# Kernel tuning notes

Measured on AMD Instinct MI355X. Metric: run time of the kernel, lower is better.

Reference implementation:

```python
import jax, jax.numpy as jnp
import numpy as np

NF = 64            # n_filter
CFAC = 3           # SinSobel c_factor: identity + sobel-x + sobel-y
FIN = NF * CFAC    # dyna block input channels (192)
FH = NF * 2        # dyna hidden (128)
FOUT = NF          # dyna output (64)
LAT = 512
N_CALLS = 6        # ceil(log2(128) - log2(2))
P_SIZES = [FH * FIN, FH, FH * FH, FH, FOUT * FH, FOUT, FOUT * FIN, FOUT]
P_TOTAL = sum(P_SIZES)  # 61824
_OFFS = np.cumsum([0] + P_SIZES)

def act(t):
    return jax.nn.leaky_relu(t, 0.2)

def conv1x1(x, w, b):
    # x [B,I,H,W], w [O,I] -> [B,O,H,W]
    return jnp.einsum('bihw,oi->bohw', x, w) + b[None, :, None, None]

def res_block(x, w0, b0, w1, b1):
    # GAN-stability style residual block with 1x1 convs
    return x + 0.1 * conv1x1(act(conv1x1(act(x), w0, b0)), w1, b1)

def depthwise3x3(x, k2d):
    C = x.shape[1]
    k = jnp.broadcast_to(k2d.astype(x.dtype), (C, 1, 3, 3))
    return jax.lax.conv_general_dilated(
        x, k, (1, 1), [(1, 1), (1, 1)],
        dimension_numbers=('NCHW', 'OIHW', 'NCHW'),
        feature_group_count=C)

SOBEL_X = jnp.array([[1., 0., -1.], [2., 0., -2.], [1., 0., -1.]], jnp.float32) / 8.0
SOBEL_Y = SOBEL_X.T
_g = jnp.exp(-0.5 * jnp.array([-1., 0., 1.], jnp.float32) ** 2)
GAUSS = jnp.outer(_g, _g)
GAUSS = GAUSS / GAUSS.sum()

def sin_sobel(x):
    return jnp.concatenate([x, depthwise3x3(x, SOBEL_X), depthwise3x3(x, SOBEL_Y)], axis=1)

def dyna_residual(x, params):
    # per-sample hypernetwork-generated 1x1-conv residual block
    B = x.shape[0]
    def take(i, shape):
        return params[:, _OFFS[i]:_OFFS[i + 1]].reshape((B,) + shape)
    w_in, b_in = take(0, (FH, FIN)), take(1, (FH,))
    w_mid, b_mid = take(2, (FH, FH)), take(3, (FH,))
    w_out, b_out = take(4, (FOUT, FH)), take(5, (FOUT,))
    w_sk, b_sk = take(6, (FOUT, FIN)), take(7, (FOUT,))
    def pconv(h, w, b):  # batched per-sample 1x1 conv
        return jnp.einsum('bihw,boi->bohw', h, w) + b[:, :, None, None]
    x_s = pconv(x, w_sk, b_sk)
    dx = pconv(x, w_in, b_in)
    dx = pconv(act(dx), w_mid, b_mid)
    dx = pconv(act(dx), w_out, b_out)
    return x_s + dx

def downsample(x):
    # GaussianSmoothing(k=3, sigma=1, pad=1) then bilinear 0.5
    # (align_corners=False bilinear at scale 0.5 == 2x2 average pooling)
    x = depthwise3x3(x, GAUSS)
    B, C, H, W = x.shape
    return x.reshape(B, C, H // 2, 2, W // 2, 2).mean(axis=(3, 5))

def lin_res(x, w1, b1, w2, b2, sw=None, sb=None):
    x_s = x if sw is None else x @ sw + sb
    return x_s + 0.1 * (act(act(x) @ w1 + b1) @ w2 + b2)

def forward(x, inj_lat, leak, in_w, in_b, inrb_w0, inrb_b0, inrb_w1, inrb_b1,
            hyp_w, hyp_b, outrb_w0, outrb_b0, outrb_w1, outrb_b1,
            l1_sw, l1_sb, l1_w1, l1_b1, l1_w2, l1_b2,
            l2_w1, l2_b1, l2_w2, l2_b2, lo_w, lo_b):
    out = conv1x1(x, in_w, in_b)
    out = res_block(out, inrb_w0, inrb_b0, inrb_w1, inrb_b1)
    leak_f = jnp.clip(leak, 0.001, 1000.0)
    dyn_params = inj_lat @ hyp_w + hyp_b  # [B, P_TOTAL], shared across calls
    out_embs = [out]
    for _ in range(N_CALLS):  # fixed small layer loop; spatial dims halve each call
        out_new = sin_sobel(out)
        out_new = dyna_residual(out_new, dyn_params)
        out = out + leak_f * out_new
        out = downsample(out)
        out_embs.append(out)
    out = res_block(out, outrb_w0, outrb_b0, outrb_w1, outrb_b1)
    h = out.mean(axis=(2, 3))  # [B, NF]
    h = lin_res(h, l1_w1, l1_b1, l1_w2, l1_b2, l1_sw, l1_sb)
    h = lin_res(h, l2_w1, l2_b1, l2_w2, l2_b2)
    lat = h @ lo_w + lo_b
    return lat, out_embs

def setup_inputs() -> dict:
    key = jax.random.key(0)
    ks = jax.random.split(key, 24)
    B, C, S = 8, 3, 128
    def rn(k, shape, scale=0.05):
        return scale * jax.random.normal(k, shape, jnp.float32)
    z = lambda n: jnp.zeros((n,), jnp.float32)
    return {
        'x': jax.random.normal(ks[0], (B, C, S, S), jnp.float32),
        'inj_lat': jax.random.normal(ks[1], (B, LAT), jnp.float32),
        'leak': jnp.array(0.1, jnp.float32),
        'in_w': rn(ks[2], (NF, C)), 'in_b': z(NF),
        'inrb_w0': rn(ks[3], (NF, NF)), 'inrb_b0': z(NF),
        'inrb_w1': rn(ks[4], (NF, NF)), 'inrb_b1': z(NF),
        'hyp_w': rn(ks[5], (LAT, P_TOTAL), 0.01), 'hyp_b': rn(ks[6], (P_TOTAL,), 0.01),
        'outrb_w0': rn(ks[7], (NF, NF)), 'outrb_b0': z(NF),
        'outrb_w1': rn(ks[8], (NF, NF)), 'outrb_b1': z(NF),
        'l1_sw': rn(ks[9], (NF, LAT)), 'l1_sb': z(LAT),
        'l1_w1': rn(ks[10], (NF, 2 * LAT)), 'l1_b1': z(2 * LAT),
        'l1_w2': rn(ks[11], (2 * LAT, LAT)), 'l1_b2': z(LAT),
        'l2_w1': rn(ks[12], (LAT, LAT)), 'l2_b1': z(LAT),
        'l2_w2': rn(ks[13], (LAT, LAT)), 'l2_b2': z(LAT),
        'lo_w': rn(ks[14], (LAT, LAT)), 'lo_b': z(LAT),
    }

def reference(x, inj_lat, leak, in_w, in_b, inrb_w0, inrb_b0, inrb_w1, inrb_b1,
              hyp_w, hyp_b, outrb_w0, outrb_b0, outrb_w1, outrb_b1,
              l1_sw, l1_sb, l1_w1, l1_b1, l1_w2, l1_b2,
              l2_w1, l2_b1, l2_w2, l2_b2, lo_w, lo_b):
    lat, out_embs = forward(x, inj_lat, leak, in_w, in_b, inrb_w0, inrb_b0, inrb_w1, inrb_b1,
                            hyp_w, hyp_b, outrb_w0, outrb_b0, outrb_w1, outrb_b1,
                            l1_sw, l1_sb, l1_w1, l1_b1, l1_w2, l1_b2,
                            l2_w1, l2_b1, l2_w2, l2_b2, lo_w, lo_b)
    return (lat, *out_embs)
```

## Files before the change

kernel.cpp:

```cpp
#include <hip/hip_runtime.h>


#define BATCH 8
#define PT 61824

typedef __attribute__((ext_vector_type(8))) short bf16x8;
typedef __attribute__((ext_vector_type(4))) float f32x4;

__device__ __forceinline__ float lrelu(float v) { return v > 0.f ? v : 0.2f * v; }

__device__ __forceinline__ unsigned cvt_pk_bf16(float lo, float hi) {
    unsigned r;
    asm("v_cvt_pk_bf16_f32 %0, %1, %2" : "=v"(r) : "v"(lo), "v"(hi));
    return r;
}
__device__ __forceinline__ short f2bf1(float f) {
    unsigned r;
    asm("v_cvt_pk_bf16_f32 %0, %1, %1" : "=v"(r) : "v"(f));
    return (short)r;
}

__global__ __launch_bounds__(256) void hyper_kernel(
    const float* __restrict__ inj, const float* __restrict__ hw,
    const float* __restrict__ hb, float* __restrict__ dyn,
    short* __restrict__ dyn16)
{
    __shared__ float s_l[512 * 8];
    __shared__ float s_part[3 * 8 * 64];
    int t = threadIdx.x;
    for (int i = t; i < 4096; i += 256) {
        int b = i >> 9, k = i & 511;
        s_l[k * 8 + b] = inj[i];
    }
    __syncthreads();
    int po = t & 63, kq = t >> 6;
    int p = blockIdx.x * 64 + po;
    float acc[8];
#pragma unroll
    for (int b = 0; b < 8; ++b) acc[b] = 0.f;
    for (int k = kq * 128; k < kq * 128 + 128; ++k) {
        float w = hw[(size_t)k * PT + p];
        float4 a0 = *(const float4*)&s_l[k * 8];
        float4 a1 = *(const float4*)&s_l[k * 8 + 4];
        acc[0] += a0.x * w; acc[1] += a0.y * w; acc[2] += a0.z * w; acc[3] += a0.w * w;
        acc[4] += a1.x * w; acc[5] += a1.y * w; acc[6] += a1.z * w; acc[7] += a1.w * w;
    }
    if (kq > 0) {
#pragma unroll
        for (int b = 0; b < 8; ++b) s_part[((kq - 1) * 8 + b) * 64 + po] = acc[b];
    }
    __syncthreads();
    if (kq == 0) {
        float bias = hb[p];
        bool isb = (p >= 24576 && p < 24704) || (p >= 41088 && p < 41216)
                || (p >= 49408 && p < 49472) || (p >= 61760);
#pragma unroll
        for (int b = 0; b < 8; ++b) {
            float v = acc[b] + s_part[b * 64 + po] + s_part[(8 + b) * 64 + po]
                    + s_part[(16 + b) * 64 + po] + bias;
            if (isb) dyn[(size_t)b * PT + p] = v;
            dyn16[(size_t)b * PT + p] = f2bf1(v);
        }
    }
}

__global__ __launch_bounds__(256) void stem_kernel(
    const float* __restrict__ x, const float* __restrict__ in_w,
    const float* __restrict__ in_b,
    const float* __restrict__ w0, const float* __restrict__ b0,
    const float* __restrict__ w1, const float* __restrict__ b1,
    float* __restrict__ out0)
{
    const int HW = 128 * 128;
    __shared__ float s_t0[64 * 68];
    __shared__ short s_vh[2 * 64 * 72];
    __shared__ float s_x[192];
    short* s_v = s_vh;
    short* s_h = s_vh + 64 * 72;
    float* s_y = (float*)s_vh;

    const int b = blockIdx.x >> 8;
    const int tile = blockIdx.x & 255;
    const int pix0 = tile * 64;
    const int t = threadIdx.x;
    const int l = t & 63, w = t >> 6;
    const int lp = l & 15, lq = l >> 4;

    if (t < 192) s_x[t] = x[(size_t)b * 3 * HW + (t >> 6) * HW + pix0 + (t & 63)];
    __syncthreads();

    for (int j = t; j < 1024; j += 256) {
        int p = j & 63, cg = j >> 6;
        float x0 = s_x[p], x1 = s_x[64 + p], x2 = s_x[128 + p];
        short pk[4];
#pragma unroll
        for (int cc = 0; cc < 4; ++cc) {
            int c = cg * 4 + cc;
            float v = in_b[c] + x0 * in_w[c * 3] + x1 * in_w[c * 3 + 1]
                    + x2 * in_w[c * 3 + 2];
            s_t0[c * 68 + p] = v;
            pk[cc] = f2bf1(lrelu(v));
        }
        *(short4*)&s_v[p * 72 + cg * 4] = make_short4(pk[0], pk[1], pk[2], pk[3]);
    }
    __syncthreads();

    const int o = w * 16 + lp;
    const f32x4 z4 = {0.f, 0.f, 0.f, 0.f};

    bf16x8 wb0[2], wb1[2];
#pragma unroll
    for (int k = 0; k < 2; ++k) {
        bf16x8 p0, p1;
#pragma unroll
        for (int e = 0; e < 8; ++e) {
            p0[e] = f2bf1(w0[o * 64 + k * 32 + lq * 8 + e]);
            p1[e] = f2bf1(w1[o * 64 + k * 32 + lq * 8 + e]);
        }
        wb0[k] = p0; wb1[k] = p1;
    }

    {
        float bi = b0[o];
        f32x4 acc[4];
#pragma unroll
        for (int mt = 0; mt < 4; ++mt) acc[mt] = z4;
#pragma unroll
        for (int k = 0; k < 2; ++k)
#pragma unroll
            for (int mt = 0; mt < 4; ++mt) {
                bf16x8 a = *(const bf16x8*)&s_v[(mt * 16 + lp) * 72 + k * 32 + lq * 8];
                acc[mt] = __builtin_amdgcn_mfma_f32_16x16x32_bf16(a, wb0[k], acc[mt], 0, 0, 0);
            }
#pragma unroll
        for (int mt = 0; mt < 4; ++mt)
#pragma unroll
            for (int r = 0; r < 4; ++r)
                s_h[(mt * 16 + lq * 4 + r) * 72 + o] = f2bf1(lrelu(acc[mt][r] + bi));
    }
    __syncthreads();

    {
        float bi = b1[o];
        f32x4 acc[4];
#pragma unroll
        for (int mt = 0; mt < 4; ++mt) acc[mt] = z4;
#pragma unroll
        for (int k = 0; k < 2; ++k)
#pragma unroll
            for (int mt = 0; mt < 4; ++mt) {
                bf16x8 a = *(const bf16x8*)&s_h[(mt * 16 + lp) * 72 + k * 32 + lq * 8];
                acc[mt] = __builtin_amdgcn_mfma_f32_16x16x32_bf16(a, wb1[k], acc[mt], 0, 0, 0);
            }
        __syncthreads();
#pragma unroll
        for (int mt = 0; mt < 4; ++mt) {
            f32x4 dv;
#pragma unroll
            for (int r = 0; r < 4; ++r) dv[r] = 0.1f * (acc[mt][r] + bi);
            *(f32x4*)&s_y[o * 68 + mt * 16 + lq * 4] = dv;
        }
    }
    __syncthreads();

#pragma unroll
    for (int v = 0; v < 4; ++v) {
        int idx = v * 1024 + t * 4;
        int oo = idx >> 6, px = idx & 63;
        f32x4 t0v = *(const f32x4*)&s_t0[oo * 68 + px];
        f32x4 dv = *(const f32x4*)&s_y[oo * 68 + px];
        f32x4 ov = t0v + dv;
        *(f32x4*)&out0[((size_t)b * 64 + oo) * HW + pix0 + px] = ov;
    }
}

template<int MT>
__global__ __launch_bounds__(256)
__attribute__((amdgpu_waves_per_eu(4, 4)))
void iter_kernel(
    const float* __restrict__ cur, const float* __restrict__ dynf,
    const short* __restrict__ dynb, const float* __restrict__ leak_p,
    float* __restrict__ y, int S, int sh)
{
    constexpr int PX = MT * 16;
    constexpr int SY = (MT == 4) ? 68 : 20;
    __shared__ short s_s[PX * 192];
    __shared__ short s_h[PX * 128];
    float* s_y = (float*)s_s;

    const int HW = S * S;
    const int tilesPer = HW / PX;
    const int nwg = BATCH * tilesPer;
    const int rb = (int)blockIdx.x;
    const int lb = (rb & 7) * (nwg >> 3) + (rb >> 3);
    const int b = lb / tilesPer;
    const int tile = lb - b * tilesPer;
    const int pix0 = tile * PX;
    const int t = threadIdx.x;
    const int l = t & 63, w = t >> 6;
    const int lp = l & 15, lq = l >> 4;
    const float* base = cur + (size_t)b * 64 * HW;
    const float lk = fminf(fmaxf(leak_p[0], 0.001f), 1000.f);

    if constexpr (MT == 4) {
        const int p = lp + 16 * w;
        const int rxw = (p & 7) << 2;
        const int gpx = pix0 + p;
        const int row = gpx >> sh;
        const int x = gpx & (S - 1);
        const bool rm = (row > 0), rp = (row < S - 1);
        float* halo_a = (float*)s_h;
        float* halo_d = halo_a + 640;
        int* s32 = (int*)s_s;

        float vm[16], vv[16], vp[16];
        const float* col = base + row * S + x;
#pragma unroll
        for (int j = 0; j < 16; ++j) {
            const int c = 2 * (lq + 4 * (j >> 1)) + (j & 1);
            const float* ch = col + (size_t)c * HW;
            vm[j] = rm ? ch[-S] : 0.f;
            vv[j] = ch[0];
            vp[j] = rp ? ch[S] : 0.f;
        }
        __builtin_amdgcn_sched_barrier(0);
        float a[16], d[16];
#pragma unroll
        for (int j = 0; j < 16; ++j) {
            a[j] = vm[j] + 2.f * vv[j] + vp[j];
            d[j] = vm[j] - vp[j];
        }
        if (w == 0 || w == 3) {
            const bool left = (w == 0) && (lp == 0);
            const bool right = (w == 3) && (lp == 15);
            if (left || right) {
                const int xe = left ? x - 1 : x + 1;
                const int slot = left ? 8 : 9;
                const bool valid = (xe >= 0) && (xe < S);
                const float* ecol = base + row * S + xe;
#pragma unroll
                for (int j = 0; j < 16; ++j) {
                    const int c = 2 * (lq + 4 * (j >> 1)) + (j & 1);
                    float em = 0.f, e0 = 0.f, ep = 0.f;
                    if (valid) {
                        const float* ch = ecol + (size_t)c * HW;
                        em = rm ? ch[-S] : 0.f;
                        e0 = ch[0];
                        ep = rp ? ch[S] : 0.f;
                    }
                    halo_a[slot * 64 + c] = em + 2.f * e0 + ep;
                    halo_d[slot * 64 + c] = em - ep;
                }
            }
        }
        if (lp == 0 || lp == 15) {
            const int slot = 2 * w + (lp == 15 ? 1 : 0);
#pragma unroll
            for (int j = 0; j < 16; ++j) {
                const int c = 2 * (lq + 4 * (j >> 1)) + (j & 1);
                halo_a[slot * 64 + c] = a[j];
                halo_d[slot * 64 + c] = d[j];
            }
        }
        __syncthreads();
        const int slotL = (w == 0) ? 8 : 2 * (w - 1) + 1;
        const int slotR = (w == 3) ? 9 : 2 * (w + 1);
#pragma unroll
        for (int i = 0; i < 8; ++i) {
            float sx2[2], sy2[2];
#pragma unroll
            for (int cc = 0; cc < 2; ++cc) {
                const int j = 2 * i + cc;
                const int c = 2 * (lq + 4 * i) + cc;
                float aL = __shfl(a[j], l - 1), dL = __shfl(d[j], l - 1);
                float aR = __shfl(a[j], l + 1), dR = __shfl(d[j], l + 1);
                if (lp == 0)  { aL = halo_a[slotL * 64 + c]; dL = halo_d[slotL * 64 + c]; }
                if (lp == 15) { aR = halo_a[slotR * 64 + c]; dR = halo_d[slotR * 64 + c]; }
                if (x == 0)     { aL = 0.f; dL = 0.f; }
                if (x == S - 1) { aR = 0.f; dR = 0.f; }
                sx2[cc] = (aL - aR) * 0.125f;
                sy2[cc] = (dL + 2.f * d[j] + dR) * 0.125f;
            }
            const int cp = lq + 4 * i;
            const int cpx_ = cp ^ rxw;
            s32[p * 96 + cpx_] = (int)cvt_pk_bf16(vv[2 * i], vv[2 * i + 1]);
            s32[p * 96 + 32 + cpx_] = (int)cvt_pk_bf16(sx2[0], sx2[1]);
            s32[p * 96 + 64 + cpx_] = (int)cvt_pk_bf16(sy2[0], sy2[1]);
        }
    } else {
        const int p = lp;
        const int rxw = (p & 7) << 2;
        const int gpx = pix0 + p;
        const int row = gpx >> sh;
        const int x = gpx & (S - 1);
        const bool rm = (row > 0), rp = (row < S - 1);
        const bool le = (lp == 0) && (x > 0);
        const bool re = (lp == 15) && (x < S - 1);
        int* s32 = (int*)s_s;
#pragma unroll
        for (int i = 0; i < 2; ++i) {
            const int cp = lq + 4 * w + 16 * i;
            float v0s[2], sxs[2], sys[2];
#pragma unroll
            for (int cc = 0; cc < 2; ++cc) {
                const int c = 2 * cp + cc;
                const float* ch = base + (size_t)c * HW + row * S;
                float vm = rm ? ch[x - S] : 0.f;
                float v0 = ch[x];
                float vp = rp ? ch[x + S] : 0.f;
                float elm = 0.f, el0 = 0.f, elp = 0.f, erm = 0.f, er0 = 0.f, erp = 0.f;
                if (le) { elm = rm ? ch[x - 1 - S] : 0.f; el0 = ch[x - 1]; elp = rp ? ch[x - 1 + S] : 0.f; }
                if (re) { erm = rm ? ch[x + 1 - S] : 0.f; er0 = ch[x + 1]; erp = rp ? ch[x + 1 + S] : 0.f; }
                float Lm = __shfl(vm, l - 1), L0 = __shfl(v0, l - 1), Lp = __shfl(vp, l - 1);
                float Rm = __shfl(vm, l + 1), R0 = __shfl(v0, l + 1), Rp = __shfl(vp, l + 1);
                if (lp == 0)  { Lm = elm; L0 = el0; Lp = elp; }
                if (lp == 15) { Rm = erm; R0 = er0; Rp = erp; }
                if (x == 0)     { Lm = 0.f; L0 = 0.f; Lp = 0.f; }
                if (x == S - 1) { Rm = 0.f; R0 = 0.f; Rp = 0.f; }
                v0s[cc] = v0;
                sxs[cc] = (Lm - Rm + 2.f * (L0 - R0) + Lp - Rp) * 0.125f;
                sys[cc] = (Lm + 2.f * vm + Rm - Lp - 2.f * vp - Rp) * 0.125f;
            }
            const int cpx_ = cp ^ rxw;
            s32[p * 96 + cpx_] = (int)cvt_pk_bf16(v0s[0], v0s[1]);
            s32[p * 96 + 32 + cpx_] = (int)cvt_pk_bf16(sxs[0], sxs[1]);
            s32[p * 96 + 64 + cpx_] = (int)cvt_pk_bf16(sys[0], sys[1]);
        }
    }
    __syncthreads();

    const short* wb = dynb + (size_t)b * PT;
    const float* pf = dynf + (size_t)b * PT;
    const f32x4 z4 = {0.f, 0.f, 0.f, 0.f};
    const int sx4 = (lp & 7) << 4;
    const char* ss_b = (const char*)s_s;
    const char* sh_cb = (const char*)s_h;
    char* sh_b = (char*)s_h;

    f32x4 acc_sk[MT];
#pragma unroll
    for (int mt = 0; mt < MT; ++mt) acc_sk[mt] = z4;

    {
        const float bi0 = pf[24576 + (w * 2) * 16 + lp];
        const float bi1 = pf[24576 + (w * 2 + 1) * 16 + lp];
        f32x4 acc[2][MT];
#pragma unroll
        for (int n = 0; n < 2; ++n)
#pragma unroll
            for (int mt = 0; mt < MT; ++mt) acc[n][mt] = z4;
        const int osk = w * 16 + lp;
        __builtin_amdgcn_s_setprio(1);
#pragma unroll 2
        for (int k = 0; k < 6; ++k) {
            bf16x8 a[MT];
#pragma unroll
            for (int mt = 0; mt < MT; ++mt)
                a[mt] = *(const bf16x8*)(ss_b + (mt * 16 + lp) * 384 + ((k * 64 + lq * 16) ^ sx4));
#pragma unroll
            for (int n = 0; n < 2; ++n) {
                int o = (w * 2 + n) * 16 + lp;
                bf16x8 bb = *(const bf16x8*)&wb[o * 192 + k * 32 + lq * 8];
#pragma unroll
                for (int mt = 0; mt < MT; ++mt)
                    acc[n][mt] = __builtin_amdgcn_mfma_f32_16x16x32_bf16(a[mt], bb, acc[n][mt], 0, 0, 0);
            }
            {
                bf16x8 bsk = *(const bf16x8*)&wb[49472 + osk * 192 + k * 32 + lq * 8];
#pragma unroll
                for (int mt = 0; mt < MT; ++mt)
                    acc_sk[mt] = __builtin_amdgcn_mfma_f32_16x16x32_bf16(a[mt], bsk, acc_sk[mt], 0, 0, 0);
            }
        }
        __builtin_amdgcn_s_setprio(0);
#pragma unroll
        for (int n = 0; n < 2; ++n) {
            int o = (w * 2 + n) * 16 + lp;
            float bi = n ? bi1 : bi0;
#pragma unroll
            for (int mt = 0; mt < MT; ++mt)
#pragma unroll
                for (int r = 0; r < 4; ++r) {
                    int row = mt * 16 + lq * 4 + r;
                    *(short*)(sh_b + row * 256 + ((o * 2) ^ ((row & 7) << 4))) =
                        f2bf1(lrelu(acc[n][mt][r] + bi));
                }
        }
    }
    __syncthreads();

    {
        const float bi0 = pf[41088 + (w * 2) * 16 + lp];
        const float bi1 = pf[41088 + (w * 2 + 1) * 16 + lp];
        f32x4 acc[2][MT];
#pragma unroll
        for (int n = 0; n < 2; ++n)
#pragma unroll
            for (int mt = 0; mt < MT; ++mt) acc[n][mt] = z4;
#pragma unroll 2
        for (int k = 0; k < 4; ++k) {
            bf16x8 a[MT];
#pragma unroll
            for (int mt = 0; mt < MT; ++mt)
                a[mt] = *(const bf16x8*)(sh_cb + (mt * 16 + lp) * 256 + ((k * 64 + lq * 16) ^ sx4));
#pragma unroll
            for (int n = 0; n < 2; ++n) {
                int o = (w * 2 + n) * 16 + lp;
                bf16x8 bb = *(const bf16x8*)&wb[24704 + o * 128 + k * 32 + lq * 8];
#pragma unroll
                for (int mt = 0; mt < MT; ++mt)
                    acc[n][mt] = __builtin_amdgcn_mfma_f32_16x16x32_bf16(a[mt], bb, acc[n][mt], 0, 0, 0);
            }
        }
        __syncthreads();
#pragma unroll
        for (int n = 0; n < 2; ++n) {
            int o = (w * 2 + n) * 16 + lp;
            float bi = n ? bi1 : bi0;
#pragma unroll
            for (int mt = 0; mt < MT; ++mt)
#pragma unroll
                for (int r = 0; r < 4; ++r) {
                    int row = mt * 16 + lq * 4 + r;
                    *(short*)(sh_b + row * 256 + ((o * 2) ^ ((row & 7) << 4))) =
                        f2bf1(lrelu(acc[n][mt][r] + bi));
                }
        }
    }
    __syncthreads();

    {
        int o = w * 16 + lp;
        const float bi = pf[49408 + o] + pf[61760 + o];
        f32x4 acc[MT];
#pragma unroll
        for (int mt = 0; mt < MT; ++mt) acc[mt] = acc_sk[mt];
#pragma unroll 2
        for (int k = 0; k < 4; ++k) {
            bf16x8 bb = *(const bf16x8*)&wb[41216 + o * 128 + k * 32 + lq * 8];
#pragma unroll
            for (int mt = 0; mt < MT; ++mt) {
                bf16x8 a = *(const bf16x8*)(sh_cb + (mt * 16 + lp) * 256 + ((k * 64 + lq * 16) ^ sx4));
                acc[mt] = __builtin_amdgcn_mfma_f32_16x16x32_bf16(a, bb, acc[mt], 0, 0, 0);
            }
        }
#pragma unroll
        for (int mt = 0; mt < MT; ++mt) {
            f32x4 dv;
#pragma unroll
            for (int r = 0; r < 4; ++r) dv[r] = acc[mt][r] + bi;
            *(f32x4*)&s_y[o * SY + mt * 16 + lq * 4] = dv;
        }
    }
    __syncthreads();

    {
        if (MT == 4) {
#pragma unroll
            for (int v = 0; v < 4; ++v) {
                int idx = v * 1024 + t * 4;
                int o = idx >> 6, px = idx & 63;
                f32x4 sv = *(const f32x4*)&s_y[o * SY + px];
                const float* cb = cur + ((size_t)b * 64 + o) * HW + pix0 + px;
                float* yb = y + ((size_t)b * 64 + o) * HW + pix0 + px;
                f32x4 cv = *(const f32x4*)cb;
                *(f32x4*)yb = cv + lk * sv;
            }
        } else {
            int o = t >> 2, px = (t & 3) * 4;
            f32x4 sv = *(const f32x4*)&s_y[o * SY + px];
            const float* cb = cur + ((size_t)b * 64 + o) * HW + pix0 + px;
            float* yb = y + ((size_t)b * 64 + o) * HW + pix0 + px;
            f32x4 cv = *(const f32x4*)cb;
            *(f32x4*)yb = cv + lk * sv;
        }
    }
}

__global__ __launch_bounds__(256) void down_kernel(
    const float* __restrict__ yin, float* __restrict__ outp,
    int S, int S2, int TW, int CPB, int tiles)
{
    __shared__ float s_in[3072];
    __shared__ float s_hb[1152];

    const float ga = 0.60653065971263342f;
    const float gs = 1.f / ((1.f + 2.f * ga) * (1.f + 2.f * ga));
    const float u0 = ga, u1 = 1.f + ga;

    const int t = threadIdx.x;
    const int nwg = (int)gridDim.x;
    const int rb = (int)blockIdx.x;
    const int bi = (rb & 7) * (nwg >> 3) + (rb >> 3);
    const int tix = bi % tiles;
    const int rem = bi / tiles;
    const int tiy = rem % tiles;
    const int cg = rem / tiles;
    const int bc0 = cg * CPB;

    const int IH = 2 * TW + 2;
    const int IW = IH;
    const int IWP = IW + 2;
    const int HS = TW + 1;
    const int gy0 = tiy * 2 * TW - 1;
    const int gx0 = tix * 2 * TW - 1;

    const int loadTot = CPB * IH * IW;
    for (int j = t; j < loadTot; j += 256) {
        int c = j / (IH * IW);
        int r = j - c * (IH * IW);
        int iy = r / IW, ix = r - iy * IW;
        int gy = gy0 + iy, gx = gx0 + ix;
        float v = 0.f;
        if (gy >= 0 && gy < S && gx >= 0 && gx < S)
            v = yin[(size_t)(bc0 + c) * S * S + gy * S + gx];
        s_in[(c * IH + iy) * IWP + ix] = v;
    }
    __syncthreads();

    const int hTot = CPB * IH * TW;
    for (int j = t; j < hTot; j += 256) {
        int c = j / (IH * TW);
        int r = j - c * (IH * TW);
        int iy = r / TW, ox = r - iy * TW;
        const float* pin = &s_in[(c * IH + iy) * IWP + 2 * ox];
        s_hb[(c * IH + iy) * HS + ox] =
            u0 * (pin[0] + pin[3]) + u1 * (pin[1] + pin[2]);
    }
    __syncthreads();

    {
        int ox = t % TW;
        int r = t / TW;
        int oy = r % TW;
        int c = r / TW;
        const float* ph = &s_hb[(c * IH + 2 * oy) * HS + ox];
        float acc = u0 * (ph[0] + ph[3 * HS]) + u1 * (ph[HS] + ph[2 * HS]);
        outp[(size_t)(bc0 + c) * S2 * S2 + (tiy * TW + oy) * S2 + tix * TW + ox] =
            acc * 0.25f * gs;
    }
}

__global__ __launch_bounds__(256) void head_a_kernel(
    const float* __restrict__ emb6,
    const float* __restrict__ w0, const float* __restrict__ b0,
    const float* __restrict__ w1, const float* __restrict__ b1,
    float* __restrict__ h)
{
    __shared__ float sm_t[256], sm_v[256], sm_r[256];
    int b = blockIdx.x, t = threadIdx.x;
    sm_t[t] = emb6[b * 256 + t];
    __syncthreads();
    {
        int o = t & 63, p = t >> 6;
        float acc = 0.f;
        for (int k = 0; k < 64; ++k) acc += w0[o * 64 + k] * lrelu(sm_t[k * 4 + p]);
        sm_v[o * 4 + p] = lrelu(acc + b0[o]);
    }
    __syncthreads();
    {
        int o = t & 63, p = t >> 6;
        float acc = 0.f;
        for (int k = 0; k < 64; ++k) acc += w1[o * 64 + k] * sm_v[k * 4 + p];
        sm_r[o * 4 + p] = sm_t[o * 4 + p] + 0.1f * (acc + b1[o]);
    }
    __syncthreads();
    if (t < 64)
        h[b * 64 + t] = 0.25f * (sm_r[t * 4] + sm_r[t * 4 + 1] + sm_r[t * 4 + 2] + sm_r[t * 4 + 3]);
}

__global__ __launch_bounds__(256) void head_b_kernel(
    const float* __restrict__ h, const float* __restrict__ w,
    const float* __restrict__ bias, float* __restrict__ t1)
{
    __shared__ float s_h[64];
    int id = blockIdx.x * 256 + threadIdx.x;
    int b = id >> 10, o = id & 1023;
    if (threadIdx.x < 64) s_h[threadIdx.x] = lrelu(h[b * 64 + threadIdx.x]);
    __syncthreads();
    float acc = 0.f;
    for (int k = 0; k < 64; ++k) acc += s_h[k] * w[k * 1024 + o];
    t1[b * 1024 + o] = lrelu(acc + bias[o]);
}

__global__ __launch_bounds__(256) void head_c_kernel(
    const float* __restrict__ h, const float* __restrict__ t1,
    const float* __restrict__ sw, const float* __restrict__ sb,
    const float* __restrict__ w2, const float* __restrict__ b2,
    float* __restrict__ h1)
{
    __shared__ float s_t[8 * 128];
    __shared__ float s_h[8 * 64];
    int oblk = blockIdx.x & 1, chunk = blockIdx.x >> 1;
    int t = threadIdx.x;
    int o = oblk * 256 + t;
    for (int j = t; j < 1024; j += 256) {
        int b = j >> 7, kk = j & 127;
        s_t[j] = t1[b * 1024 + chunk * 128 + kk];
    }
    if (chunk == 0)
        for (int j = t; j < 512; j += 256) s_h[j] = h[j];
    __syncthreads();
    float acc[8];
#pragma unroll
    for (int b = 0; b < 8; ++b) acc[b] = 0.f;
    for (int kk = 0; kk < 128; ++kk) {
        float wv = w2[(chunk * 128 + kk) * 512 + o];
#pragma unroll
        for (int b = 0; b < 8; ++b) acc[b] += s_t[b * 128 + kk] * wv;
    }
#pragma unroll
    for (int b = 0; b < 8; ++b) acc[b] *= 0.1f;
    if (chunk == 0) {
        for (int k = 0; k < 64; ++k) {
            float wv = sw[k * 512 + o];
#pragma unroll
            for (int b = 0; b < 8; ++b) acc[b] += s_h[b * 64 + k] * wv;
        }
        float c0 = sb[o] + 0.1f * b2[o];
#pragma unroll
        for (int b = 0; b < 8; ++b) acc[b] += c0;
    }
#pragma unroll
    for (int b = 0; b < 8; ++b) atomicAdd(&h1[b * 512 + o], acc[b]);
}

__global__ __launch_bounds__(256) void head_d_kernel(
    const float* __restrict__ h1, const float* __restrict__ w,
    const float* __restrict__ bias, float* __restrict__ z3)
{
    __shared__ float s_u[8 * 64];
    int oblk = blockIdx.x & 1, chunk = blockIdx.x >> 1;
    int t = threadIdx.x;
    int o = oblk * 256 + t;
    for (int j = t; j < 512; j += 256) {
        int b = j >> 6, kk = j & 63;
        s_u[j] = lrelu(h1[b * 512 + chunk * 64 + kk]);
    }
    __syncthreads();
    float acc[8];
#pragma unroll
    for (int b = 0; b < 8; ++b) acc[b] = 0.f;
    for (int kk = 0; kk < 64; ++kk) {
        float wv = w[(chunk * 64 + kk) * 512 + o];
#pragma unroll
        for (int b = 0; b < 8; ++b) acc[b] += s_u[b * 64 + kk] * wv;
    }
    if (chunk == 0) {
        float c0 = bias[o];
#pragma unroll
        for (int b = 0; b < 8; ++b) acc[b] += c0;
    }
#pragma unroll
    for (int b = 0; b < 8; ++b) atomicAdd(&z3[b * 512 + o], acc[b]);
}

__global__ __launch_bounds__(256) void head_e_kernel(
    const float* __restrict__ h1, const float* __restrict__ z3,
    const float* __restrict__ w, const float* __restrict__ bias,
    float* __restrict__ h2)
{
    __shared__ float s_u[8 * 64];
    int oblk = blockIdx.x & 1, chunk = blockIdx.x >> 1;
    int t = threadIdx.x;
    int o = oblk * 256 + t;
    for (int j = t; j < 512; j += 256) {
        int b = j >> 6, kk = j & 63;
        s_u[j] = lrelu(z3[b * 512 + chunk * 64 + kk]);
    }
    __syncthreads();
    float acc[8];
#pragma unroll
    for (int b = 0; b < 8; ++b) acc[b] = 0.f;
    for (int kk = 0; kk < 64; ++kk) {
        float wv = w[(chunk * 64 + kk) * 512 + o];
#pragma unroll
        for (int b = 0; b < 8; ++b) acc[b] += s_u[b * 64 + kk] * wv;
    }
#pragma unroll
    for (int b = 0; b < 8; ++b) acc[b] *= 0.1f;
    if (chunk == 0) {
        float c0 = 0.1f * bias[o];
#pragma unroll
        for (int b = 0; b < 8; ++b) acc[b] += h1[b * 512 + o] + c0;
    }
#pragma unroll
    for (int b = 0; b < 8; ++b) atomicAdd(&h2[b * 512 + o], acc[b]);
}

__global__ __launch_bounds__(256) void head_f_kernel(
    const float* __restrict__ h2, const float* __restrict__ w,
    const float* __restrict__ bias, float* __restrict__ lat)
{
    __shared__ float s_u[8 * 64];
    int oblk = blockIdx.x & 1, chunk = blockIdx.x >> 1;
    int t = threadIdx.x;
    int o = oblk * 256 + t;
    for (int j = t; j < 512; j += 256) {
        int b = j >> 6, kk = j & 63;
        s_u[j] = h2[b * 512 + chunk * 64 + kk];
    }
    __syncthreads();
    float acc[8];
#pragma unroll
    for (int b = 0; b < 8; ++b) acc[b] = 0.f;
    for (int kk = 0; kk < 64; ++kk) {
        float wv = w[(chunk * 64 + kk) * 512 + o];
#pragma unroll
        for (int b = 0; b < 8; ++b) acc[b] += s_u[b * 64 + kk] * wv;
    }
    if (chunk == 0) {
        float c0 = bias[o];
#pragma unroll
        for (int b = 0; b < 8; ++b) acc[b] += c0;
    }
#pragma unroll
    for (int b = 0; b < 8; ++b) atomicAdd(&lat[b * 512 + o], acc[b]);
}

extern "C" void kernel_launch(void* const* d_in, const int* in_sizes, int n_in,
                              void* d_out, int out_size, void* d_ws, size_t ws_size,
                              hipStream_t stream) {
    const float* x      = (const float*)d_in[0];
    const float* inj    = (const float*)d_in[1];
    const float* leak   = (const float*)d_in[2];
    const float* in_w   = (const float*)d_in[3];
    const float* in_b   = (const float*)d_in[4];
    const float* inrb_w0 = (const float*)d_in[5];
    const float* inrb_b0 = (const float*)d_in[6];
    const float* inrb_w1 = (const float*)d_in[7];
    const float* inrb_b1 = (const float*)d_in[8];
    const float* hyp_w  = (const float*)d_in[9];
    const float* hyp_b  = (const float*)d_in[10];
    const float* outrb_w0 = (const float*)d_in[11];
    const float* outrb_b0 = (const float*)d_in[12];
    const float* outrb_w1 = (const float*)d_in[13];
    const float* outrb_b1 = (const float*)d_in[14];
    const float* l1_sw  = (const float*)d_in[15];
    const float* l1_sb  = (const float*)d_in[16];
    const float* l1_w1  = (const float*)d_in[17];
    const float* l1_b1  = (const float*)d_in[18];
    const float* l1_w2  = (const float*)d_in[19];
    const float* l1_b2  = (const float*)d_in[20];
    const float* l2_w1  = (const float*)d_in[21];
    const float* l2_b1  = (const float*)d_in[22];
    const float* l2_w2  = (const float*)d_in[23];
    const float* l2_b2  = (const float*)d_in[24];
    const float* lo_w   = (const float*)d_in[25];
    const float* lo_b   = (const float*)d_in[26];

    float* out = (float*)d_out;
    float* dyn = (float*)d_ws;
    float* ybuf = dyn + (size_t)BATCH * PT;
    short* dyn16 = (short*)(ybuf + (size_t)BATCH * 64 * 16384);
    float* hbuf = (float*)(dyn16 + (size_t)BATCH * PT);
    float* t1buf = hbuf + 512;
    float* h1buf = t1buf + 8192;
    float* z3buf = h1buf + 4096;
    float* h2buf = z3buf + 4096;

    hipMemsetAsync(h1buf, 0, (4096 * 3) * sizeof(float), stream);
    hipMemsetAsync(out, 0, 4096 * sizeof(float), stream);

    hyper_kernel<<<PT / 64, 256, 0, stream>>>(inj, hyp_w, hyp_b, dyn, dyn16);

    size_t cur = 4096;
    stem_kernel<<<BATCH * 256, 256, 0, stream>>>(
        x, in_w, in_b, inrb_w0, inrb_b0, inrb_w1, inrb_b1, out + cur);

    int S = 128, sh = 7;
    for (int i = 0; i < 6; ++i) {
        if (S >= 8) {
            iter_kernel<4><<<BATCH * (S * S / 64), 256, 0, stream>>>(
                out + cur, dyn, dyn16, leak, ybuf, S, sh);
        } else {
            iter_kernel<1><<<BATCH * (S * S / 16), 256, 0, stream>>>(
                out + cur, dyn, dyn16, leak, ybuf, S, sh);
        }
        int S2 = S >> 1;
        size_t nxt = cur + (size_t)BATCH * 64 * S * S;
        int TW = (S2 >= 16) ? 16 : S2;
        int tiles = S2 / TW;
        int CPB = 256 / (TW * TW);
        if (CPB < 1) CPB = 1;
        int grid = (BATCH * 64 / CPB) * tiles * tiles;
        down_kernel<<<grid, 256, 0, stream>>>(ybuf, out + nxt, S, S2, TW, CPB, tiles);
        cur = nxt;
        S = S2; sh -= 1;
    }

    head_a_kernel<<<BATCH, 256, 0, stream>>>(
        out + cur, outrb_w0, outrb_b0, outrb_w1, outrb_b1, hbuf);
    head_b_kernel<<<32, 256, 0, stream>>>(hbuf, l1_w1, l1_b1, t1buf);
    head_c_kernel<<<16, 256, 0, stream>>>(hbuf, t1buf, l1_sw, l1_sb, l1_w2, l1_b2, h1buf);
    head_d_kernel<<<16, 256, 0, stream>>>(h1buf, l2_w1, l2_b1, z3buf);
    head_e_kernel<<<16, 256, 0, stream>>>(h1buf, z3buf, l2_w2, l2_b2, h2buf);
    head_f_kernel<<<16, 256, 0, stream>>>(h2buf, lo_w, lo_b, out);
}
```

Measured before the change: 509.8 us.

## Merge hyper and stem kernels; fuse small-scale iterations and head into tail kernel

```diff
diff --git a/kernel.cpp b/kernel.cpp
--- a/kernel.cpp
+++ b/kernel.cpp
@@ -20,187 +20,22 @@
     return (short)r;
 }
 
-__global__ __launch_bounds__(256) void hyper_kernel(
-    const float* __restrict__ inj, const float* __restrict__ hw,
-    const float* __restrict__ hb, float* __restrict__ dyn,
-    short* __restrict__ dyn16)
-{
-    __shared__ float s_l[512 * 8];
-    __shared__ float s_part[3 * 8 * 64];
-    int t = threadIdx.x;
-    for (int i = t; i < 4096; i += 256) {
-        int b = i >> 9, k = i & 511;
-        s_l[k * 8 + b] = inj[i];
-    }
-    __syncthreads();
-    int po = t & 63, kq = t >> 6;
-    int p = blockIdx.x * 64 + po;
-    float acc[8];
-#pragma unroll
-    for (int b = 0; b < 8; ++b) acc[b] = 0.f;
-    for (int k = kq * 128; k < kq * 128 + 128; ++k) {
-        float w = hw[(size_t)k * PT + p];
-        float4 a0 = *(const float4*)&s_l[k * 8];
-        float4 a1 = *(const float4*)&s_l[k * 8 + 4];
-        acc[0] += a0.x * w; acc[1] += a0.y * w; acc[2] += a0.z * w; acc[3] += a0.w * w;
-        acc[4] += a1.x * w; acc[5] += a1.y * w; acc[6] += a1.z * w; acc[7] += a1.w * w;
-    }
-    if (kq > 0) {
-#pragma unroll
-        for (int b = 0; b < 8; ++b) s_part[((kq - 1) * 8 + b) * 64 + po] = acc[b];
-    }
-    __syncthreads();
-    if (kq == 0) {
-        float bias = hb[p];
-        bool isb = (p >= 24576 && p < 24704) || (p >= 41088 && p < 41216)
-                || (p >= 49408 && p < 49472) || (p >= 61760);
-#pragma unroll
-        for (int b = 0; b < 8; ++b) {
-            float v = acc[b] + s_part[b * 64 + po] + s_part[(8 + b) * 64 + po]
-                    + s_part[(16 + b) * 64 + po] + bias;
-            if (isb) dyn[(size_t)b * PT + p] = v;
-            dyn16[(size_t)b * PT + p] = f2bf1(v);
-        }
-    }
-}
-
-__global__ __launch_bounds__(256) void stem_kernel(
-    const float* __restrict__ x, const float* __restrict__ in_w,
-    const float* __restrict__ in_b,
-    const float* __restrict__ w0, const float* __restrict__ b0,
-    const float* __restrict__ w1, const float* __restrict__ b1,
-    float* __restrict__ out0)
-{
-    const int HW = 128 * 128;
-    __shared__ float s_t0[64 * 68];
-    __shared__ short s_vh[2 * 64 * 72];
-    __shared__ float s_x[192];
-    short* s_v = s_vh;
-    short* s_h = s_vh + 64 * 72;
-    float* s_y = (float*)s_vh;
-
-    const int b = blockIdx.x >> 8;
-    const int tile = blockIdx.x & 255;
-    const int pix0 = tile * 64;
-    const int t = threadIdx.x;
-    const int l = t & 63, w = t >> 6;
-    const int lp = l & 15, lq = l >> 4;
-
-    if (t < 192) s_x[t] = x[(size_t)b * 3 * HW + (t >> 6) * HW + pix0 + (t & 63)];
-    __syncthreads();
-
-    for (int j = t; j < 1024; j += 256) {
-        int p = j & 63, cg = j >> 6;
-        float x0 = s_x[p], x1 = s_x[64 + p], x2 = s_x[128 + p];
-        short pk[4];
-#pragma unroll
-        for (int cc = 0; cc < 4; ++cc) {
-            int c = cg * 4 + cc;
-            float v = in_b[c] + x0 * in_w[c * 3] + x1 * in_w[c * 3 + 1]
-                    + x2 * in_w[c * 3 + 2];
-            s_t0[c * 68 + p] = v;
-            pk[cc] = f2bf1(lrelu(v));
-        }
-        *(short4*)&s_v[p * 72 + cg * 4] = make_short4(pk[0], pk[1], pk[2], pk[3]);
-    }
-    __syncthreads();
-
-    const int o = w * 16 + lp;
-    const f32x4 z4 = {0.f, 0.f, 0.f, 0.f};
-
-    bf16x8 wb0[2], wb1[2];
-#pragma unroll
-    for (int k = 0; k < 2; ++k) {
-        bf16x8 p0, p1;
-#pragma unroll
-        for (int e = 0; e < 8; ++e) {
-            p0[e] = f2bf1(w0[o * 64 + k * 32 + lq * 8 + e]);
-            p1[e] = f2bf1(w1[o * 64 + k * 32 + lq * 8 + e]);
-        }
-        wb0[k] = p0; wb1[k] = p1;
-    }
-
-    {
-        float bi = b0[o];
-        f32x4 acc[4];
-#pragma unroll
-        for (int mt = 0; mt < 4; ++mt) acc[mt] = z4;
-#pragma unroll
-        for (int k = 0; k < 2; ++k)
-#pragma unroll
-            for (int mt = 0; mt < 4; ++mt) {
-                bf16x8 a = *(const bf16x8*)&s_v[(mt * 16 + lp) * 72 + k * 32 + lq * 8];
-                acc[mt] = __builtin_amdgcn_mfma_f32_16x16x32_bf16(a, wb0[k], acc[mt], 0, 0, 0);
-            }
-#pragma unroll
-        for (int mt = 0; mt < 4; ++mt)
-#pragma unroll
-            for (int r = 0; r < 4; ++r)
-                s_h[(mt * 16 + lq * 4 + r) * 72 + o] = f2bf1(lrelu(acc[mt][r] + bi));
-    }
-    __syncthreads();
-
-    {
-        float bi = b1[o];
-        f32x4 acc[4];
-#pragma unroll
-        for (int mt = 0; mt < 4; ++mt) acc[mt] = z4;
-#pragma unroll
-        for (int k = 0; k < 2; ++k)
-#pragma unroll
-            for (int mt = 0; mt < 4; ++mt) {
-                bf16x8 a = *(const bf16x8*)&s_h[(mt * 16 + lp) * 72 + k * 32 + lq * 8];
-                acc[mt] = __builtin_amdgcn_mfma_f32_16x16x32_bf16(a, wb1[k], acc[mt], 0, 0, 0);
-            }
-        __syncthreads();
-#pragma unroll
-        for (int mt = 0; mt < 4; ++mt) {
-            f32x4 dv;
-#pragma unroll
-            for (int r = 0; r < 4; ++r) dv[r] = 0.1f * (acc[mt][r] + bi);
-            *(f32x4*)&s_y[o * 68 + mt * 16 + lq * 4] = dv;
-        }
-    }
-    __syncthreads();
-
-#pragma unroll
-    for (int v = 0; v < 4; ++v) {
-        int idx = v * 1024 + t * 4;
-        int oo = idx >> 6, px = idx & 63;
-        f32x4 t0v = *(const f32x4*)&s_t0[oo * 68 + px];
-        f32x4 dv = *(const f32x4*)&s_y[oo * 68 + px];
-        f32x4 ov = t0v + dv;
-        *(f32x4*)&out0[((size_t)b * 64 + oo) * HW + pix0 + px] = ov;
-    }
-}
-
 template<int MT>
-__global__ __launch_bounds__(256)
-__attribute__((amdgpu_waves_per_eu(4, 4)))
-void iter_kernel(
+__device__ void iter_tile(
+    int b, int pix0, int S, int sh,
     const float* __restrict__ cur, const float* __restrict__ dynf,
-    const short* __restrict__ dynb, const float* __restrict__ leak_p,
-    float* __restrict__ y, int S, int sh)
-{
-    constexpr int PX = MT * 16;
+    const short* __restrict__ dynb, float lk, float* __restrict__ y,
+    short* s_s, short* s_h)
+{
     constexpr int SY = (MT == 4) ? 68 : 20;
-    __shared__ short s_s[PX * 192];
-    __shared__ short s_h[PX * 128];
-    float* s_y = (float*)s_s;
-
     const int HW = S * S;
-    const int tilesPer = HW / PX;
-    const int nwg = BATCH * tilesPer;
-    const int rb = (int)blockIdx.x;
-    const int lb = (rb & 7) * (nwg >> 3) + (rb >> 3);
-    const int b = lb / tilesPer;
-    const int tile = lb - b * tilesPer;
-    const int pix0 = tile * PX;
     const int t = threadIdx.x;
     const int l = t & 63, w = t >> 6;
     const int lp = l & 15, lq = l >> 4;
     const float* base = cur + (size_t)b * 64 * HW;
-    const float lk = fminf(fmaxf(leak_p[0], 0.001f), 1000.f);
+    float* s_y = (float*)s_s;
+
+    __syncthreads();
 
     if constexpr (MT == 4) {
         const int p = lp + 16 * w;
@@ -223,7 +58,6 @@
             vv[j] = ch[0];
             vp[j] = rp ? ch[S] : 0.f;
         }
-        __builtin_amdgcn_sched_barrier(0);
         float a[16], d[16];
 #pragma unroll
         for (int j = 0; j < 16; ++j) {
@@ -350,7 +184,6 @@
 #pragma unroll
             for (int mt = 0; mt < MT; ++mt) acc[n][mt] = z4;
         const int osk = w * 16 + lp;
-        __builtin_amdgcn_s_setprio(1);
 #pragma unroll 2
         for (int k = 0; k < 6; ++k) {
             bf16x8 a[MT];
@@ -372,7 +205,6 @@
                     acc_sk[mt] = __builtin_amdgcn_mfma_f32_16x16x32_bf16(a[mt], bsk, acc_sk[mt], 0, 0, 0);
             }
         }
-        __builtin_amdgcn_s_setprio(0);
 #pragma unroll
         for (int n = 0; n < 2; ++n) {
             int o = (w * 2 + n) * 16 + lp;
@@ -455,25 +287,299 @@
     __syncthreads();
 
     {
+        const int HW2 = HW;
         if (MT == 4) {
 #pragma unroll
             for (int v = 0; v < 4; ++v) {
                 int idx = v * 1024 + t * 4;
                 int o = idx >> 6, px = idx & 63;
                 f32x4 sv = *(const f32x4*)&s_y[o * SY + px];
-                const float* cb = cur + ((size_t)b * 64 + o) * HW + pix0 + px;
-                float* yb = y + ((size_t)b * 64 + o) * HW + pix0 + px;
+                const float* cb = cur + ((size_t)b * 64 + o) * HW2 + pix0 + px;
+                float* yb = y + ((size_t)b * 64 + o) * HW2 + pix0 + px;
                 f32x4 cv = *(const f32x4*)cb;
                 *(f32x4*)yb = cv + lk * sv;
             }
         } else {
             int o = t >> 2, px = (t & 3) * 4;
             f32x4 sv = *(const f32x4*)&s_y[o * SY + px];
-            const float* cb = cur + ((size_t)b * 64 + o) * HW + pix0 + px;
-            float* yb = y + ((size_t)b * 64 + o) * HW + pix0 + px;
+            const float* cb = cur + ((size_t)b * 64 + o) * HW2 + pix0 + px;
+            float* yb = y + ((size_t)b * 64 + o) * HW2 + pix0 + px;
             f32x4 cv = *(const f32x4*)cb;
             *(f32x4*)yb = cv + lk * sv;
         }
+    }
+}
+
+__global__ __launch_bounds__(256) void hs_kernel(
+    const float* __restrict__ inj, const float* __restrict__ hw,
+    const float* __restrict__ hb, float* __restrict__ dyn,
+    short* __restrict__ dyn16,
+    const float* __restrict__ x, const float* __restrict__ in_w,
+    const float* __restrict__ in_b,
+    const float* __restrict__ w0, const float* __restrict__ b0,
+    const float* __restrict__ w1, const float* __restrict__ b1,
+    float* __restrict__ out0)
+{
+    __shared__ float smem[9216];
+    const int bid = (int)blockIdx.x;
+    const int t = threadIdx.x;
+
+    if (bid < 966) {
+        float* s_l = smem;
+        float* s_part = s_l + 4096;
+        for (int i = t; i < 4096; i += 256) {
+            int b = i >> 9, k = i & 511;
+            s_l[k * 8 + b] = inj[i];
+        }
+        __syncthreads();
+        int po = t & 63, kq = t >> 6;
+        int p = bid * 64 + po;
+        float acc[8];
+#pragma unroll
+        for (int b = 0; b < 8; ++b) acc[b] = 0.f;
+        for (int k = kq * 128; k < kq * 128 + 128; ++k) {
+            float w = hw[(size_t)k * PT + p];
+            float4 a0 = *(const float4*)&s_l[k * 8];
+            float4 a1 = *(const float4*)&s_l[k * 8 + 4];
+            acc[0] += a0.x * w; acc[1] += a0.y * w; acc[2] += a0.z * w; acc[3] += a0.w * w;
+            acc[4] += a1.x * w; acc[5] += a1.y * w; acc[6] += a1.z * w; acc[7] += a1.w * w;
+        }
+        if (kq > 0) {
+#pragma unroll
+            for (int b = 0; b < 8; ++b) s_part[((kq - 1) * 8 + b) * 64 + po] = acc[b];
+        }
+        __syncthreads();
+        if (kq == 0) {
+            float bias = hb[p];
+            bool isb = (p >= 24576 && p < 24704) || (p >= 41088 && p < 41216)
+                    || (p >= 49408 && p < 49472) || (p >= 61760);
+#pragma unroll
+            for (int b = 0; b < 8; ++b) {
+                float v = acc[b] + s_part[b * 64 + po] + s_part[(8 + b) * 64 + po]
+                        + s_part[(16 + b) * 64 + po] + bias;
+                if (isb) dyn[(size_t)b * PT + p] = v;
+                dyn16[(size_t)b * PT + p] = f2bf1(v);
+            }
+        }
+        return;
+    }
+
+    const int HW = 128 * 128;
+    float* s_t0 = smem;
+    short* s_vh = (short*)(s_t0 + 64 * 68);
+    float* s_x = (float*)(s_vh + 2 * 64 * 72);
+    short* s_v = s_vh;
+    short* s_h = s_vh + 64 * 72;
+    float* s_y = (float*)s_vh;
+
+    const int sb = bid - 966;
+    const int b = sb >> 8;
+    const int tile = sb & 255;
+    const int pix0 = tile * 64;
+    const int l = t & 63, w = t >> 6;
+    const int lp = l & 15, lq = l >> 4;
+
+    if (t < 192) s_x[t] = x[(size_t)b * 3 * HW + (t >> 6) * HW + pix0 + (t & 63)];
+    __syncthreads();
+
+    for (int j = t; j < 1024; j += 256) {
+        int p = j & 63, cg = j >> 6;
+        float x0 = s_x[p], x1 = s_x[64 + p], x2 = s_x[128 + p];
+        short pk[4];
+#pragma unroll
+        for (int cc = 0; cc < 4; ++cc) {
+            int c = cg * 4 + cc;
+            float v = in_b[c] + x0 * in_w[c * 3] + x1 * in_w[c * 3 + 1]
+                    + x2 * in_w[c * 3 + 2];
+            s_t0[c * 68 + p] = v;
+            pk[cc] = f2bf1(lrelu(v));
+        }
+        *(short4*)&s_v[p * 72 + cg * 4] = make_short4(pk[0], pk[1], pk[2], pk[3]);
+    }
+    __syncthreads();
+
+    const int o = w * 16 + lp;
+    const f32x4 z4 = {0.f, 0.f, 0.f, 0.f};
+
+    bf16x8 wb0[2], wb1[2];
+#pragma unroll
+    for (int k = 0; k < 2; ++k) {
+        bf16x8 p0, p1;
+#pragma unroll
+        for (int e = 0; e < 8; ++e) {
+            p0[e] = f2bf1(w0[o * 64 + k * 32 + lq * 8 + e]);
+            p1[e] = f2bf1(w1[o * 64 + k * 32 + lq * 8 + e]);
+        }
+        wb0[k] = p0; wb1[k] = p1;
+    }
+
+    {
+        float bi = b0[o];
+        f32x4 acc[4];
+#pragma unroll
+        for (int mt = 0; mt < 4; ++mt) acc[mt] = z4;
+#pragma unroll
+        for (int k = 0; k < 2; ++k)
+#pragma unroll
+            for (int mt = 0; mt < 4; ++mt) {
+                bf16x8 a = *(const bf16x8*)&s_v[(mt * 16 + lp) * 72 + k * 32 + lq * 8];
+                acc[mt] = __builtin_amdgcn_mfma_f32_16x16x32_bf16(a, wb0[k], acc[mt], 0, 0, 0);
+            }
+#pragma unroll
+        for (int mt = 0; mt < 4; ++mt)
+#pragma unroll
+            for (int r = 0; r < 4; ++r)
+                s_h[(mt * 16 + lq * 4 + r) * 72 + o] = f2bf1(lrelu(acc[mt][r] + bi));
+    }
+    __syncthreads();
+
+    {
+        float bi = b1[o];
+        f32x4 acc[4];
+#pragma unroll
+        for (int mt = 0; mt < 4; ++mt) acc[mt] = z4;
+#pragma unroll
+        for (int k = 0; k < 2; ++k)
+#pragma unroll
+            for (int mt = 0; mt < 4; ++mt) {
+                bf16x8 a = *(const bf16x8*)&s_h[(mt * 16 + lp) * 72 + k * 32 + lq * 8];
+                acc[mt] = __builtin_amdgcn_mfma_f32_16x16x32_bf16(a, wb1[k], acc[mt], 0, 0, 0);
+            }
+        __syncthreads();
+#pragma unroll
+        for (int mt = 0; mt < 4; ++mt) {
+            f32x4 dv;
+#pragma unroll
+            for (int r = 0; r < 4; ++r) dv[r] = 0.1f * (acc[mt][r] + bi);
+            *(f32x4*)&s_y[o * 68 + mt * 16 + lq * 4] = dv;
+        }
+    }
+    __syncthreads();
+
+#pragma unroll
+    for (int v = 0; v < 4; ++v) {
+        int idx = v * 1024 + t * 4;
+        int oo = idx >> 6, px = idx & 63;
+        f32x4 t0v = *(const f32x4*)&s_t0[oo * 68 + px];
+        f32x4 dv = *(const f32x4*)&s_y[oo * 68 + px];
+        f32x4 ov = t0v + dv;
+        *(f32x4*)&out0[((size_t)b * 64 + oo) * HW + pix0 + px] = ov;
+    }
+}
+
+template<int MT>
+__global__ __launch_bounds__(256) void iter_kernel(
+    const float* __restrict__ cur, const float* __restrict__ dynf,
+    const short* __restrict__ dynb, const float* __restrict__ leak_p,
+    float* __restrict__ y, int S, int sh)
+{
+    constexpr int PX = MT * 16;
+    __shared__ short s_s[PX * 192];
+    __shared__ short s_h[PX * 128];
+
+    const int tilesPer = S * S / PX;
+    const int nwg = BATCH * tilesPer;
+    const int rb = (int)blockIdx.x;
+    const int lb = (rb & 7) * (nwg >> 3) + (rb >> 3);
+    const int b = lb / tilesPer;
+    const int tile = lb - b * tilesPer;
+    const float lk = fminf(fmaxf(leak_p[0], 0.001f), 1000.f);
+
+    iter_tile<MT>(b, tile * PX, S, sh, cur, dynf, dynb, lk, y, s_s, s_h);
+}
+
+__device__ void down_tile(int b, int S, const float* __restrict__ src,
+                          float* __restrict__ dst, float* sm_opt)
+{
+    __syncthreads();
+    const int S2 = S >> 1;
+    const float ga = 0.60653065971263342f;
+    const float gs = 1.f / ((1.f + 2.f * ga) * (1.f + 2.f * ga));
+    const float u0 = ga, u1 = 1.f + ga;
+    const int tot = 64 * S2 * S2;
+    for (int idx = threadIdx.x; idx < tot; idx += 256) {
+        int c = idx / (S2 * S2);
+        int r = idx - c * (S2 * S2);
+        int oy = r / S2, ox = r - oy * S2;
+        const float* sp = src + (size_t)(b * 64 + c) * S * S;
+        float hrow[4];
+#pragma unroll
+        for (int dy = 0; dy < 4; ++dy) {
+            int ay = 2 * oy - 1 + dy;
+            if (ay < 0 || ay >= S) { hrow[dy] = 0.f; continue; }
+            int ax0 = 2 * ox - 1;
+            float p0 = (ax0 >= 0) ? sp[ay * S + ax0] : 0.f;
+            float p1 = sp[ay * S + ax0 + 1];
+            float p2 = sp[ay * S + ax0 + 2];
+            float p3 = (ax0 + 3 < S) ? sp[ay * S + ax0 + 3] : 0.f;
+            hrow[dy] = u0 * (p0 + p3) + u1 * (p1 + p2);
+        }
+        float acc = u0 * (hrow[0] + hrow[3]) + u1 * (hrow[1] + hrow[2]);
+        float val = acc * 0.25f * gs;
+        dst[(size_t)(b * 64 + c) * S2 * S2 + oy * S2 + ox] = val;
+        if (sm_opt) sm_opt[idx] = val;
+    }
+}
+
+__global__ __launch_bounds__(256) void tail_kernel(
+    const float* __restrict__ emb3, float* __restrict__ emb4,
+    float* __restrict__ emb5, float* __restrict__ emb6,
+    const float* __restrict__ dynf, const short* __restrict__ dynb,
+    const float* __restrict__ leak_p, float* __restrict__ ybuf,
+    const float* __restrict__ aw0, const float* __restrict__ ab0,
+    const float* __restrict__ aw1, const float* __restrict__ ab1,
+    const float* __restrict__ l1w1, const float* __restrict__ l1b1,
+    float* __restrict__ hbuf, float* __restrict__ t1buf)
+{
+    __shared__ short s_s[64 * 192];
+    __shared__ short s_h[64 * 128];
+    const int b = (int)blockIdx.x;
+    const int t = threadIdx.x;
+    const float lk = fminf(fmaxf(leak_p[0], 0.001f), 1000.f);
+
+    for (int tile = 0; tile < 4; ++tile)
+        iter_tile<4>(b, tile * 64, 16, 4, emb3, dynf, dynb, lk, ybuf, s_s, s_h);
+    down_tile(b, 16, ybuf, emb4, nullptr);
+
+    iter_tile<4>(b, 0, 8, 3, emb4, dynf, dynb, lk, ybuf, s_s, s_h);
+    down_tile(b, 8, ybuf, emb5, nullptr);
+
+    float* sm_t = (float*)s_h;
+    float* sm_v = sm_t + 256;
+    float* sm_r = sm_v + 256;
+    iter_tile<1>(b, 0, 4, 2, emb5, dynf, dynb, lk, ybuf, s_s, s_h);
+    __syncthreads();
+    down_tile(b, 4, ybuf, emb6, sm_t);
+    __syncthreads();
+
+    {
+        int o = t & 63, p = t >> 6;
+        float acc = 0.f;
+        for (int k = 0; k < 64; ++k) acc += aw0[o * 64 + k] * lrelu(sm_t[k * 4 + p]);
+        sm_v[o * 4 + p] = lrelu(acc + ab0[o]);
+    }
+    __syncthreads();
+    {
+        int o = t & 63, p = t >> 6;
+        float acc = 0.f;
+        for (int k = 0; k < 64; ++k) acc += aw1[o * 64 + k] * sm_v[k * 4 + p];
+        sm_r[o * 4 + p] = sm_t[o * 4 + p] + 0.1f * (acc + ab1[o]);
+    }
+    __syncthreads();
+    float* ah = sm_v;
+    if (t < 64) {
+        float hv = 0.25f * (sm_r[t * 4] + sm_r[t * 4 + 1] + sm_r[t * 4 + 2] + sm_r[t * 4 + 3]);
+        hbuf[b * 64 + t] = hv;
+        ah[t] = lrelu(hv);
+    }
+    __syncthreads();
+
+#pragma unroll
+    for (int j = 0; j < 4; ++j) {
+        int o = t + 256 * j;
+        float acc = 0.f;
+        for (int k = 0; k < 64; ++k) acc += ah[k] * l1w1[k * 1024 + o];
+        t1buf[b * 1024 + o] = lrelu(acc + l1b1[o]);
     }
 }
 
@@ -539,48 +645,6 @@
         outp[(size_t)(bc0 + c) * S2 * S2 + (tiy * TW + oy) * S2 + tix * TW + ox] =
             acc * 0.25f * gs;
     }
-}
-
-__global__ __launch_bounds__(256) void head_a_kernel(
-    const float* __restrict__ emb6,
-    const float* __restrict__ w0, const float* __restrict__ b0,
-    const float* __restrict__ w1, const float* __restrict__ b1,
-    float* __restrict__ h)
-{
-    __shared__ float sm_t[256], sm_v[256], sm_r[256];
-    int b = blockIdx.x, t = threadIdx.x;
-    sm_t[t] = emb6[b * 256 + t];
-    __syncthreads();
-    {
-        int o = t & 63, p = t >> 6;
-        float acc = 0.f;
-        for (int k = 0; k < 64; ++k) acc += w0[o * 64 + k] * lrelu(sm_t[k * 4 + p]);
-        sm_v[o * 4 + p] = lrelu(acc + b0[o]);
-    }
-    __syncthreads();
-    {
-        int o = t & 63, p = t >> 6;
-        float acc = 0.f;
-        for (int k = 0; k < 64; ++k) acc += w1[o * 64 + k] * sm_v[k * 4 + p];
-        sm_r[o * 4 + p] = sm_t[o * 4 + p] + 0.1f * (acc + b1[o]);
-    }
-    __syncthreads();
-    if (t < 64)
-        h[b * 64 + t] = 0.25f * (sm_r[t * 4] + sm_r[t * 4 + 1] + sm_r[t * 4 + 2] + sm_r[t * 4 + 3]);
-}
-
-__global__ __launch_bounds__(256) void head_b_kernel(
-    const float* __restrict__ h, const float* __restrict__ w,
-    const float* __restrict__ bias, float* __restrict__ t1)
-{
-    __shared__ float s_h[64];
-    int id = blockIdx.x * 256 + threadIdx.x;
-    int b = id >> 10, o = id & 1023;
-    if (threadIdx.x < 64) s_h[threadIdx.x] = lrelu(h[b * 64 + threadIdx.x]);
-    __syncthreads();
-    float acc = 0.f;
-    for (int k = 0; k < 64; ++k) acc += s_h[k] * w[k * 1024 + o];
-    t1[b * 1024 + o] = lrelu(acc + bias[o]);
 }
 
 __global__ __launch_bounds__(256) void head_c_kernel(
@@ -762,36 +826,35 @@
     hipMemsetAsync(h1buf, 0, (4096 * 3) * sizeof(float), stream);
     hipMemsetAsync(out, 0, 4096 * sizeof(float), stream);
 
-    hyper_kernel<<<PT / 64, 256, 0, stream>>>(inj, hyp_w, hyp_b, dyn, dyn16);
+    hs_kernel<<<966 + BATCH * 256, 256, 0, stream>>>(
+        inj, hyp_w, hyp_b, dyn, dyn16,
+        x, in_w, in_b, inrb_w0, inrb_b0, inrb_w1, inrb_b1, out + 4096);
 
     size_t cur = 4096;
-    stem_kernel<<<BATCH * 256, 256, 0, stream>>>(
-        x, in_w, in_b, inrb_w0, inrb_b0, inrb_w1, inrb_b1, out + cur);
-
     int S = 128, sh = 7;
-    for (int i = 0; i < 6; ++i) {
-        if (S >= 8) {
-            iter_kernel<4><<<BATCH * (S * S / 64), 256, 0, stream>>>(
-                out + cur, dyn, dyn16, leak, ybuf, S, sh);
-        } else {
-            iter_kernel<1><<<BATCH * (S * S / 16), 256, 0, stream>>>(
-                out + cur, dyn, dyn16, leak, ybuf, S, sh);
-        }
+    for (int i = 0; i < 3; ++i) {
+        iter_kernel<4><<<BATCH * (S * S / 64), 256, 0, stream>>>(
+            out + cur, dyn, dyn16, leak, ybuf, S, sh);
         int S2 = S >> 1;
         size_t nxt = cur + (size_t)BATCH * 64 * S * S;
-        int TW = (S2 >= 16) ? 16 : S2;
+        int TW = 16;
         int tiles = S2 / TW;
-        int CPB = 256 / (TW * TW);
-        if (CPB < 1) CPB = 1;
-        int grid = (BATCH * 64 / CPB) * tiles * tiles;
-        down_kernel<<<grid, 256, 0, stream>>>(ybuf, out + nxt, S, S2, TW, CPB, tiles);
+        int grid = (BATCH * 64) * tiles * tiles;
+        down_kernel<<<grid, 256, 0, stream>>>(ybuf, out + nxt, S, S2, TW, 1, tiles);
         cur = nxt;
         S = S2; sh -= 1;
     }
 
-    head_a_kernel<<<BATCH, 256, 0, stream>>>(
-        out + cur, outrb_w0, outrb_b0, outrb_w1, outrb_b1, hbuf);
-    head_b_kernel<<<32, 256, 0, stream>>>(hbuf, l1_w1, l1_b1, t1buf);
+    size_t e3 = cur;
+    size_t e4 = e3 + (size_t)BATCH * 64 * 256;
+    size_t e5 = e4 + (size_t)BATCH * 64 * 64;
+    size_t e6 = e5 + (size_t)BATCH * 64 * 16;
+    tail_kernel<<<BATCH, 256, 0, stream>>>(
+        out + e3, out + e4, out + e5, out + e6,
+        dyn, dyn16, leak, ybuf,
+        outrb_w0, outrb_b0, outrb_w1, outrb_b1,
+        l1_w1, l1_b1, hbuf, t1buf);
+
     head_c_kernel<<<16, 256, 0, stream>>>(hbuf, t1buf, l1_sw, l1_sb, l1_w2, l1_b2, h1buf);
     head_d_kernel<<<16, 256, 0, stream>>>(h1buf, l2_w1, l2_b1, z3buf);
     head_e_kernel<<<16, 256, 0, stream>>>(h1buf, z3buf, l2_w2, l2_b2, h2buf);
```

Measured after the change: 641.2 us. +25.8%, slower.
